# Kernel tuning notes

Hardware: AMD Instinct MI355X
Metric: run time of the kernel (lower is better)

Reference implementation:

```python
import jax, jax.numpy as jnp
import numpy as np

B, T, D, H, MLP, WIN = 4, 2048, 768, 12, 3072, 256
HD = D // H


def setup_inputs() -> dict:
    key = jax.random.key(0)
    ks = jax.random.split(key, 9)
    s = 0.02
    return {
        "x": jax.random.normal(ks[0], (B, T, D), jnp.float32),
        "in_proj_w": jax.random.normal(ks[1], (3 * D, D), jnp.float32) * s,
        "in_proj_b": jax.random.normal(ks[2], (3 * D,), jnp.float32) * s,
        "out_w": jax.random.normal(ks[3], (D, D), jnp.float32) * s,
        "out_b": jax.random.normal(ks[4], (D,), jnp.float32) * s,
        "w1": jax.random.normal(ks[5], (MLP, D), jnp.float32) * s,
        "b1": jax.random.normal(ks[6], (MLP,), jnp.float32) * s,
        "w2": jax.random.normal(ks[7], (D, MLP), jnp.float32) * s,
        "b2": jax.random.normal(ks[8], (D,), jnp.float32) * s,
        "ln1_g": jnp.ones((D,), jnp.float32),
        "ln1_b": jnp.zeros((D,), jnp.float32),
        "ln2_g": jnp.ones((D,), jnp.float32),
        "ln2_b": jnp.zeros((D,), jnp.float32),
        "window_size": WIN,
    }


def _layernorm(v, g, b, eps=1e-5):
    m = v.mean(-1, keepdims=True)
    var = ((v - m) ** 2).mean(-1, keepdims=True)
    return (v - m) / jnp.sqrt(var + eps) * g + b


def reference(x, in_proj_w, in_proj_b, out_w, out_b, w1, b1, w2, b2,
              ln1_g, ln1_b, ln2_g, ln2_b, window_size):
    Bx, Tx, Dx = x.shape
    # --- local (banded) multi-head self-attention on norm1(x) ---
    xn = _layernorm(x, ln1_g, ln1_b)
    qkv = xn @ in_proj_w.T + in_proj_b            # [B,T,3D]
    q, k, v = jnp.split(qkv, 3, axis=-1)
    to_heads = lambda t: t.reshape(Bx, Tx, H, HD).transpose(0, 2, 1, 3)  # [B,H,T,hd]
    q, k, v = to_heads(q), to_heads(k), to_heads(v)
    scale = jnp.asarray(1.0 / np.sqrt(HD), x.dtype)
    scores = jnp.einsum('bhqd,bhkd->bhqk', q, k) * scale  # [B,H,T,T]
    idx = jnp.arange(Tx)
    banned = jnp.abs(idx[:, None] - idx[None, :]) > window_size  # True = masked
    scores = jnp.where(banned, -jnp.inf, scores)
    attn = jax.nn.softmax(scores, axis=-1)
    o = jnp.einsum('bhqk,bhkd->bhqd', attn, v)
    o = o.transpose(0, 2, 1, 3).reshape(Bx, Tx, Dx)
    o = o @ out_w.T + out_b
    x = x + o
    # --- MLP block on norm2(x) ---
    xn = _layernorm(x, ln2_g, ln2_b)
    h = jax.nn.gelu(xn @ w1.T + b1, approximate=False)
    x = x + (h @ w2.T + b2)
    return x
```

## Files before the change

kernel.cpp:

```cpp
#include <hip/hip_runtime.h>
#include <hip/hip_bf16.h>

typedef __bf16 bf16;
typedef __bf16 v8bf __attribute__((ext_vector_type(8)));
typedef __bf16 v4bf __attribute__((ext_vector_type(4)));
typedef float  v4f  __attribute__((ext_vector_type(4)));

#define DEVI __device__ __forceinline__

constexpr int Bc   = 4;
constexpr int Tc   = 2048;
constexpr int Dc   = 768;
constexpr int Hc   = 12;
constexpr int HDc  = 64;
constexpr int MLPc = 3072;
constexpr int QKVc = 2304;
constexpr int BTc  = Bc * Tc;
constexpr int SPAD = 72;

DEVI float b2f(bf16 x) { return (float)x; }
DEVI bf16  f2b(float x) { return (bf16)x; }

#define GLDS(gp, lp) __builtin_amdgcn_global_load_lds( \
    (const __attribute__((address_space(1))) void*)(gp), \
    (__attribute__((address_space(3))) void*)(lp), 16, 0, 0)

__global__ __launch_bounds__(256) void cvt2_kernel(
    const float* __restrict__ s0, bf16* __restrict__ d0, int n0,
    const float* __restrict__ s1, bf16* __restrict__ d1)
{
    int i = blockIdx.x * 256 + threadIdx.x;
    const float* s; bf16* d; int j;
    if (i < n0) { s = s0; d = d0; j = i; }
    else        { s = s1; d = d1; j = i - n0; }
    float4 v = ((const float4*)s)[j];
    v4bf o = { f2b(v.x), f2b(v.y), f2b(v.z), f2b(v.w) };
    ((v4bf*)d)[j] = o;
}

__global__ __launch_bounds__(256) void ln_kernel(
    const float* __restrict__ x, const float* __restrict__ g,
    const float* __restrict__ bt, bf16* __restrict__ out)
{
    const int row = blockIdx.x;
    const int t = threadIdx.x;
    const float* xr = x + (size_t)row * Dc;
    float v[3];
    v[0] = xr[t];
    v[1] = xr[t + 256];
    v[2] = xr[t + 512];
    float s = v[0] + v[1] + v[2];
    float s2 = v[0]*v[0] + v[1]*v[1] + v[2]*v[2];
    #pragma unroll
    for (int off = 32; off > 0; off >>= 1) {
        s  += __shfl_down(s, off);
        s2 += __shfl_down(s2, off);
    }
    __shared__ float red[8];
    const int wave = t >> 6, lane = t & 63;
    if (lane == 0) { red[wave] = s; red[4 + wave] = s2; }
    __syncthreads();
    s  = red[0] + red[1] + red[2] + red[3];
    s2 = red[4] + red[5] + red[6] + red[7];
    const float mean = s * (1.0f / Dc);
    const float var  = s2 * (1.0f / Dc) - mean * mean;
    const float rstd = rsqrtf(var + 1e-5f);
    bf16* orow = out + (size_t)row * Dc;
    #pragma unroll
    for (int i = 0; i < 3; i++) {
        int c = t + i * 256;
        orow[c] = f2b((v[i] - mean) * rstd * g[c] + bt[c]);
    }
}

enum { EPI_QKV = 0, EPI_GELU_BF16 = 1, EPI_RESID_F32 = 2, EPI_ACC_F32 = 3 };

template <int EPI, int TN>
__global__ __launch_bounds__(256) void gemm_bt(
    const bf16* __restrict__ A, const bf16* __restrict__ Bw,
    const float* __restrict__ bias,
    bf16* __restrict__ Cb, float* __restrict__ Cf,
    const float* __restrict__ resf,
    int M, int N, int K, int lda, int ldb)
{
    constexpr int MI = (TN == 128) ? 4 : 2;
    __shared__ __align__(16) bf16 sA[128 * 64];
    __shared__ __align__(16) bf16 sB[TN * 64];
    const int t = threadIdx.x, wave = t >> 6, lane = t & 63;
    const int moff = (TN == 128) ? (wave & 1) * 64 : wave * 32;
    const int noff = (TN == 128) ? (wave >> 1) * 64 : 0;
    const int nx = gridDim.x, ny = gridDim.y;
    const int bid = blockIdx.y * nx + blockIdx.x;
    const int xcd = bid & 7, kk = bid >> 3;
    const int m0 = (xcd * (ny >> 3) + kk / nx) * 128;
    const int n0 = (kk % nx) * TN;
    const bf16* Ag = A + (size_t)m0 * lda;
    const bf16* Bg = Bw + (size_t)n0 * ldb;

    v4f acc[MI][4];
    #pragma unroll
    for (int i = 0; i < MI; i++)
        #pragma unroll
        for (int j = 0; j < 4; j++) acc[i][j] = (v4f)(0.0f);

    for (int k0 = 0; k0 < K; k0 += 64) {
        #pragma unroll
        for (int i = 0; i < 4; i++) {
            int c = i * 256 + t;
            int r = c >> 3, j = (c & 7) ^ (r & 7);
            GLDS(Ag + (size_t)r * lda + k0 + j * 8,
                 &sA[(i * 256 + wave * 64) * 8]);
        }
        #pragma unroll
        for (int i = 0; i < TN / 32; i++) {
            int c = i * 256 + t;
            int r = c >> 3, j = (c & 7) ^ (r & 7);
            GLDS(Bg + (size_t)r * ldb + k0 + j * 8,
                 &sB[(i * 256 + wave * 64) * 8]);
        }
        __syncthreads();
        #pragma unroll
        for (int ks = 0; ks < 2; ks++) {
            const int rq = lane >> 4, rl = lane & 15;
            v8bf a[MI], b[4];
            #pragma unroll
            for (int mi = 0; mi < MI; mi++) {
                const int row = moff + mi * 16 + rl;
                a[mi] = *(const v8bf*)&sA[row * 64 + ((ks * 4 + rq) ^ (row & 7)) * 8];
            }
            #pragma unroll
            for (int ni = 0; ni < 4; ni++) {
                const int row = noff + ni * 16 + rl;
                b[ni] = *(const v8bf*)&sB[row * 64 + ((ks * 4 + rq) ^ (row & 7)) * 8];
            }
            #pragma unroll
            for (int mi = 0; mi < MI; mi++)
                #pragma unroll
                for (int ni = 0; ni < 4; ni++)
                    acc[mi][ni] = __builtin_amdgcn_mfma_f32_16x16x32_bf16(
                        a[mi], b[ni], acc[mi][ni], 0, 0, 0);
        }
        __syncthreads();
    }

    const int rq = lane >> 4, cn = lane & 15;
    #pragma unroll
    for (int mi = 0; mi < MI; mi++)
        #pragma unroll
        for (int ni = 0; ni < 4; ni++) {
            const int col = n0 + noff + ni * 16 + cn;
            const float bv = bias ? bias[col] : 0.0f;
            if constexpr (EPI == EPI_QKV) {
                const int row0 = m0 + moff + mi * 16 + rq * 4;
                if (n0 < 2 * Dc) {
                    bf16* dst = Cb + (col < Dc ? 0 : (size_t)BTc * Dc);
                    const int cadj = col < Dc ? col : col - Dc;
                    #pragma unroll
                    for (int r = 0; r < 4; r++)
                        dst[(size_t)(row0 + r) * Dc + cadj] = f2b(acc[mi][ni][r] + bv);
                } else {
                    const int vcol = col - 2 * Dc;
                    const int hh = vcol >> 6, hd = vcol & 63;
                    const int bb = row0 >> 11, t0 = row0 & 2047;
                    v4bf pk;
                    #pragma unroll
                    for (int r = 0; r < 4; r++) pk[r] = f2b(acc[mi][ni][r] + bv);
                    *(v4bf*)(Cb + 2 * (size_t)BTc * Dc +
                             (((size_t)bb * Hc + hh) * HDc + hd) * Tc + t0) = pk;
                }
            } else {
                #pragma unroll
                for (int r = 0; r < 4; r++) {
                    const int row = m0 + moff + mi * 16 + rq * 4 + r;
                    const size_t idx = (size_t)row * N + col;
                    float vv = acc[mi][ni][r] + bv;
                    if constexpr (EPI == EPI_GELU_BF16) {
                        Cb[idx] = f2b(0.5f * vv * (1.0f + erff(vv * 0.70710678118f)));
                    } else if constexpr (EPI == EPI_RESID_F32) {
                        Cf[idx] = vv + resf[idx];
                    } else {
                        Cf[idx] = vv + Cf[idx];
                    }
                }
            }
        }
}

__global__ __launch_bounds__(256, 2) void attn_kernel(
    const bf16* __restrict__ Qb, const bf16* __restrict__ Kb,
    const bf16* __restrict__ Vt, bf16* __restrict__ o,
    const int* __restrict__ winp)
{
    const int bh = blockIdx.x, qt = blockIdx.y;
    const int b = bh / Hc, h = bh % Hc;
    const int q0 = qt * 64;
    const int win = *winp;
    const int t = threadIdx.x, wave = t >> 6, lane = t & 63;
    const int rq = lane >> 4, cn = lane & 15;
    constexpr float C1 = 0.125f * 1.44269504089f;

    __shared__ __align__(16) bf16 sQ[64 * SPAD];
    __shared__ __align__(16) bf16 sP[4][64 * SPAD];
    __shared__ float sL[4][64], sLf[64];

    const bf16* qp  = Qb + ((size_t)b * Tc + q0) * Dc + h * HDc;
    const bf16* kp  = Kb + ((size_t)b * Tc) * Dc + h * HDc;
    const bf16* vtp = Vt + (size_t)bh * HDc * Tc;

    #pragma unroll
    for (int i = 0; i < 2; i++) {
        int c = i * 256 + t;
        int r = c >> 3, c8 = (c & 7) * 8;
        *(uint4*)&sQ[r * SPAD + c8] = *(const uint4*)(qp + (size_t)r * Dc + c8);
    }
    __syncthreads();

    v4f acc_o[4][4], acc_l[4];
    #pragma unroll
    for (int mi = 0; mi < 4; mi++) {
        acc_l[mi] = (v4f)(0.0f);
        #pragma unroll
        for (int j = 0; j < 4; j++) acc_o[mi][j] = (v4f)(0.0f);
    }
    v8bf vones;
    #pragma unroll
    for (int j = 0; j < 8; j++) vones[j] = f2b(1.0f);

    const int s_lo = (q0 >= win) ? 0 : ((win - q0 + 63) >> 6);
    const int kb_hi = min(Tc - 64, q0 + win);
    const int s_hi = (kb_hi - (q0 - win)) >> 6;

    for (int s = s_lo + wave; s <= s_hi; s += 4) {
        const int kb0 = q0 - win + s * 64;

        v4f sf[4][4];
        #pragma unroll
        for (int mi = 0; mi < 4; mi++)
            #pragma unroll
            for (int ni = 0; ni < 4; ni++) sf[mi][ni] = (v4f)(0.0f);
        #pragma unroll
        for (int ks = 0; ks < 2; ks++) {
            const int kc = ks * 32 + rq * 8;
            v8bf a[4], kf[4];
            #pragma unroll
            for (int mi = 0; mi < 4; mi++)
                a[mi] = *(const v8bf*)&sQ[(mi * 16 + cn) * SPAD + kc];
            #pragma unroll
            for (int ni = 0; ni < 4; ni++)
                kf[ni] = *(const v8bf*)(kp + (size_t)(kb0 + ni * 16 + cn) * Dc + kc);
            #pragma unroll
            for (int mi = 0; mi < 4; mi++)
                #pragma unroll
                for (int ni = 0; ni < 4; ni++)
                    sf[mi][ni] = __builtin_amdgcn_mfma_f32_16x16x32_bf16(
                        a[mi], kf[ni], sf[mi][ni], 0, 0, 0);
        }

        const bool need_mask = (q0 + 63 - kb0 > win) || (kb0 + 63 - q0 > win);
        #pragma unroll
        for (int mi = 0; mi < 4; mi++)
            #pragma unroll
            for (int ni = 0; ni < 4; ni++)
                #pragma unroll
                for (int r = 0; r < 4; r++) {
                    float tt = sf[mi][ni][r] * C1;
                    if (need_mask) {
                        int qi = q0 + mi * 16 + rq * 4 + r;
                        int ki = kb0 + ni * 16 + cn;
                        int dd = qi - ki; dd = dd < 0 ? -dd : dd;
                        tt = (dd > win) ? -INFINITY : tt;
                    }
                    float p = exp2f(fminf(tt, 30.0f));
                    sP[wave][(mi * 16 + rq * 4 + r) * SPAD + ni * 16 + cn] = f2b(p);
                }

        #pragma unroll
        for (int ks = 0; ks < 2; ks++) {
            const int kc = ks * 32 + rq * 8;
            v8bf pa[4], vf[4];
            #pragma unroll
            for (int mi = 0; mi < 4; mi++)
                pa[mi] = *(const v8bf*)&sP[wave][(mi * 16 + cn) * SPAD + kc];
            #pragma unroll
            for (int nh = 0; nh < 4; nh++)
                vf[nh] = *(const v8bf*)(vtp + (size_t)(nh * 16 + cn) * Tc + kb0 + kc);
            #pragma unroll
            for (int mi = 0; mi < 4; mi++)
                acc_l[mi] = __builtin_amdgcn_mfma_f32_16x16x32_bf16(
                    pa[mi], vones, acc_l[mi], 0, 0, 0);
            #pragma unroll
            for (int mi = 0; mi < 4; mi++)
                #pragma unroll
                for (int nh = 0; nh < 4; nh++)
                    acc_o[mi][nh] = __builtin_amdgcn_mfma_f32_16x16x32_bf16(
                        pa[mi], vf[nh], acc_o[mi][nh], 0, 0, 0);
        }
    }

    if (cn == 0) {
        #pragma unroll
        for (int mi = 0; mi < 4; mi++)
            #pragma unroll
            for (int r = 0; r < 4; r++)
                sL[wave][mi * 16 + rq * 4 + r] = acc_l[mi][r];
    }
    __syncthreads();
    float* oacc = (float*)&sP[0][0];
    if (t < 64) {
        float Lv = sL[0][t] + sL[1][t] + sL[2][t] + sL[3][t];
        sLf[t] = (Lv > 0.0f) ? 1.0f / Lv : 0.0f;
    }
    #pragma unroll
    for (int w = 0; w < 4; w++) {
        if (wave == w) {
            #pragma unroll
            for (int mi = 0; mi < 4; mi++)
                #pragma unroll
                for (int r = 0; r < 4; r++) {
                    int row = mi * 16 + rq * 4 + r;
                    #pragma unroll
                    for (int nh = 0; nh < 4; nh++) {
                        float* p = &oacc[row * 64 + nh * 16 + cn];
                        if (w == 0) *p = acc_o[mi][nh][r];
                        else        *p += acc_o[mi][nh][r];
                    }
                }
        }
        __syncthreads();
    }
    bf16* ob = o + ((size_t)b * Tc + q0) * Dc + h * HDc;
    for (int i = t; i < 4096; i += 256) {
        int row = i >> 6, col = i & 63;
        ob[(size_t)row * Dc + col] = f2b(oacc[i] * sLf[row]);
    }
}

extern "C" void kernel_launch(void* const* d_in, const int* in_sizes, int n_in,
                              void* d_out, int out_size, void* d_ws, size_t ws_size,
                              hipStream_t stream)
{
    const float* x     = (const float*)d_in[0];
    const float* inw   = (const float*)d_in[1];
    const float* inb   = (const float*)d_in[2];
    const float* outw  = (const float*)d_in[3];
    const float* outb  = (const float*)d_in[4];
    const float* w1    = (const float*)d_in[5];
    const float* b1    = (const float*)d_in[6];
    const float* w2    = (const float*)d_in[7];
    const float* b2    = (const float*)d_in[8];
    const float* ln1g  = (const float*)d_in[9];
    const float* ln1b  = (const float*)d_in[10];
    const float* ln2g  = (const float*)d_in[11];
    const float* ln2b  = (const float*)d_in[12];
    const int*   winp  = (const int*)d_in[13];
    float* out = (float*)d_out;

    char* ws = (char*)d_ws;
    constexpr size_t A_OFF   = 0;
    constexpr size_t QKV_OFF = (size_t)BTc * Dc * 2;
    constexpr size_t WA_OFF  = QKV_OFF + 3 * (size_t)BTc * Dc * 2;
    constexpr size_t WS_NEED = WA_OFF + (size_t)(QKVc + Dc) * Dc * 2;
    if (ws_size < WS_NEED) return;

    bf16*  xn     = (bf16*)(ws + A_OFF);
    bf16*  qkvb   = (bf16*)(ws + QKV_OFF);
    bf16*  Qb     = qkvb;
    bf16*  Kb     = qkvb + (size_t)BTc * Dc;
    bf16*  Vt     = qkvb + 2 * (size_t)BTc * Dc;
    bf16*  hbuf   = (bf16*)(ws + QKV_OFF);
    bf16*  wmlp   = (bf16*)(ws + QKV_OFF + (size_t)BTc * (2 * Dc) * 2);
    bf16*  w1_b   = wmlp;
    bf16*  w2_b   = wmlp + (size_t)MLPc * Dc;
    bf16*  wqkv_b = (bf16*)(ws + WA_OFF);
    bf16*  wout_b = wqkv_b + (size_t)QKVc * Dc;

    constexpr int HALF = MLPc / 2;
    constexpr int NQKV4 = QKVc * Dc / 4, NOUT4 = Dc * Dc / 4;
    constexpr int NW14  = MLPc * Dc / 4, NW24  = Dc * MLPc / 4;

    cvt2_kernel<<<(NQKV4 + NOUT4) / 256, 256, 0, stream>>>(
        inw, wqkv_b, NQKV4, outw, wout_b);

    ln_kernel<<<BTc, 256, 0, stream>>>(x, ln1g, ln1b, xn);
    gemm_bt<EPI_QKV, 128><<<dim3(QKVc / 128, BTc / 128), 256, 0, stream>>>(
        xn, wqkv_b, inb, qkvb, nullptr, nullptr, BTc, QKVc, Dc, Dc, Dc);
    attn_kernel<<<dim3(Bc * Hc, Tc / 64), 256, 0, stream>>>(Qb, Kb, Vt, xn, winp);
    cvt2_kernel<<<(NW14 + NW24) / 256, 256, 0, stream>>>(
        w1, w1_b, NW14, w2, w2_b);
    gemm_bt<EPI_RESID_F32, 64><<<dim3(Dc / 64, BTc / 128), 256, 0, stream>>>(
        xn, wout_b, outb, nullptr, out, x, BTc, Dc, Dc, Dc, Dc);
    ln_kernel<<<BTc, 256, 0, stream>>>(out, ln2g, ln2b, xn);

    for (int c = 0; c < 2; c++) {
        const bf16* w1c = w1_b + (size_t)c * HALF * Dc;
        const bf16* w2c = w2_b + (size_t)c * HALF;
        gemm_bt<EPI_GELU_BF16, 128><<<dim3(HALF / 128, BTc / 128), 256, 0, stream>>>(
            xn, w1c, b1 + c * HALF, hbuf, nullptr, nullptr, BTc, HALF, Dc, Dc, Dc);
        gemm_bt<EPI_ACC_F32, 64><<<dim3(Dc / 64, BTc / 128), 256, 0, stream>>>(
            hbuf, w2c, (c == 0) ? b2 : nullptr, nullptr, out, nullptr,
            BTc, Dc, HALF, HALF, MLPc);
    }
}
```

Before: 382.8 us.

## Split attention work by query rows per wave and fold softmax scale into Q

Reworks the attention kernel so that each wave owns 16 query rows and loops over all key blocks, instead of splitting key blocks across waves. This removes the cross-wave reduction through shared memory and the block-level barriers. It computes S^T with K as the A operand so that P is written to a small per-wave XOR-swizzled LDS tile. The 1/sqrt(d)*log2e scale is folded into Q in the QKV GEMM epilogue, and launch bounds are raised to allow 4 blocks per CU. The trade-off is that K/V tiles are now reloaded from global memory by each of the four waves, raising redundant global and L2 traffic.

```diff
diff --git a/kernel.cpp b/kernel.cpp
--- a/kernel.cpp
+++ b/kernel.cpp
@@ -16,7 +16,6 @@
 constexpr int MLPc = 3072;
 constexpr int QKVc = 2304;
 constexpr int BTc  = Bc * Tc;
-constexpr int SPAD = 72;
 
 DEVI float b2f(bf16 x) { return (float)x; }
 DEVI bf16  f2b(float x) { return (bf16)x; }
@@ -155,9 +154,10 @@
                 if (n0 < 2 * Dc) {
                     bf16* dst = Cb + (col < Dc ? 0 : (size_t)BTc * Dc);
                     const int cadj = col < Dc ? col : col - Dc;
+                    const float qs = (col < Dc) ? 0.18033688011112042f : 1.0f;
                     #pragma unroll
                     for (int r = 0; r < 4; r++)
-                        dst[(size_t)(row0 + r) * Dc + cadj] = f2b(acc[mi][ni][r] + bv);
+                        dst[(size_t)(row0 + r) * Dc + cadj] = f2b((acc[mi][ni][r] + bv) * qs);
                 } else {
                     const int vcol = col - 2 * Dc;
                     const int hh = vcol >> 6, hd = vcol & 63;
@@ -186,7 +186,7 @@
         }
 }
 
-__global__ __launch_bounds__(256, 2) void attn_kernel(
+__global__ __launch_bounds__(256, 4) void attn_kernel(
     const bf16* __restrict__ Qb, const bf16* __restrict__ Kb,
     const bf16* __restrict__ Vt, bf16* __restrict__ o,
     const int* __restrict__ winp)
@@ -197,31 +197,25 @@
     const int win = *winp;
     const int t = threadIdx.x, wave = t >> 6, lane = t & 63;
     const int rq = lane >> 4, cn = lane & 15;
-    constexpr float C1 = 0.125f * 1.44269504089f;
-
-    __shared__ __align__(16) bf16 sQ[64 * SPAD];
-    __shared__ __align__(16) bf16 sP[4][64 * SPAD];
-    __shared__ float sL[4][64], sLf[64];
-
-    const bf16* qp  = Qb + ((size_t)b * Tc + q0) * Dc + h * HDc;
+    const int qw0 = q0 + wave * 16;
+
+    __shared__ __align__(16) bf16 sP[4][16 * 64];
+    bf16* const sPw = &sP[wave][0];
+    const int swz  = (cn & 7) << 1;
+    const int prow = cn << 6;
+
+    const bf16* qp  = Qb + ((size_t)b * Tc) * Dc + h * HDc;
     const bf16* kp  = Kb + ((size_t)b * Tc) * Dc + h * HDc;
     const bf16* vtp = Vt + (size_t)bh * HDc * Tc;
 
-    #pragma unroll
-    for (int i = 0; i < 2; i++) {
-        int c = i * 256 + t;
-        int r = c >> 3, c8 = (c & 7) * 8;
-        *(uint4*)&sQ[r * SPAD + c8] = *(const uint4*)(qp + (size_t)r * Dc + c8);
-    }
-    __syncthreads();
-
-    v4f acc_o[4][4], acc_l[4];
-    #pragma unroll
-    for (int mi = 0; mi < 4; mi++) {
-        acc_l[mi] = (v4f)(0.0f);
-        #pragma unroll
-        for (int j = 0; j < 4; j++) acc_o[mi][j] = (v4f)(0.0f);
-    }
+    v8bf qf[2];
+    #pragma unroll
+    for (int ks = 0; ks < 2; ks++)
+        qf[ks] = *(const v8bf*)(qp + (size_t)(qw0 + cn) * Dc + ks * 32 + rq * 8);
+
+    v4f acc_o[4], acc_l = (v4f)(0.0f);
+    #pragma unroll
+    for (int nh = 0; nh < 4; nh++) acc_o[nh] = (v4f)(0.0f);
     v8bf vones;
     #pragma unroll
     for (int j = 0; j < 8; j++) vones[j] = f2b(1.0f);
@@ -230,108 +224,66 @@
     const int kb_hi = min(Tc - 64, q0 + win);
     const int s_hi = (kb_hi - (q0 - win)) >> 6;
 
-    for (int s = s_lo + wave; s <= s_hi; s += 4) {
+    for (int s = s_lo; s <= s_hi; s++) {
         const int kb0 = q0 - win + s * 64;
 
-        v4f sf[4][4];
-        #pragma unroll
-        for (int mi = 0; mi < 4; mi++)
-            #pragma unroll
-            for (int ni = 0; ni < 4; ni++) sf[mi][ni] = (v4f)(0.0f);
+        v4f sf[4];
+        #pragma unroll
+        for (int kb = 0; kb < 4; kb++) sf[kb] = (v4f)(0.0f);
         #pragma unroll
         for (int ks = 0; ks < 2; ks++) {
             const int kc = ks * 32 + rq * 8;
-            v8bf a[4], kf[4];
-            #pragma unroll
-            for (int mi = 0; mi < 4; mi++)
-                a[mi] = *(const v8bf*)&sQ[(mi * 16 + cn) * SPAD + kc];
-            #pragma unroll
-            for (int ni = 0; ni < 4; ni++)
-                kf[ni] = *(const v8bf*)(kp + (size_t)(kb0 + ni * 16 + cn) * Dc + kc);
-            #pragma unroll
-            for (int mi = 0; mi < 4; mi++)
-                #pragma unroll
-                for (int ni = 0; ni < 4; ni++)
-                    sf[mi][ni] = __builtin_amdgcn_mfma_f32_16x16x32_bf16(
-                        a[mi], kf[ni], sf[mi][ni], 0, 0, 0);
-        }
-
-        const bool need_mask = (q0 + 63 - kb0 > win) || (kb0 + 63 - q0 > win);
-        #pragma unroll
-        for (int mi = 0; mi < 4; mi++)
-            #pragma unroll
-            for (int ni = 0; ni < 4; ni++)
-                #pragma unroll
-                for (int r = 0; r < 4; r++) {
-                    float tt = sf[mi][ni][r] * C1;
-                    if (need_mask) {
-                        int qi = q0 + mi * 16 + rq * 4 + r;
-                        int ki = kb0 + ni * 16 + cn;
-                        int dd = qi - ki; dd = dd < 0 ? -dd : dd;
-                        tt = (dd > win) ? -INFINITY : tt;
-                    }
-                    float p = exp2f(fminf(tt, 30.0f));
-                    sP[wave][(mi * 16 + rq * 4 + r) * SPAD + ni * 16 + cn] = f2b(p);
+            v8bf kf[4];
+            #pragma unroll
+            for (int kb = 0; kb < 4; kb++)
+                kf[kb] = *(const v8bf*)(kp + (size_t)(kb0 + kb * 16 + cn) * Dc + kc);
+            #pragma unroll
+            for (int kb = 0; kb < 4; kb++)
+                sf[kb] = __builtin_amdgcn_mfma_f32_16x16x32_bf16(
+                    kf[kb], qf[ks], sf[kb], 0, 0, 0);
+        }
+
+        const bool need_mask = (kb0 + 63 - qw0 > win) || (qw0 + 15 - kb0 > win);
+        const int qi = qw0 + cn;
+        #pragma unroll
+        for (int kb = 0; kb < 4; kb++) {
+            v4bf pk;
+            #pragma unroll
+            for (int r = 0; r < 4; r++) {
+                float tt = sf[kb][r];
+                if (need_mask) {
+                    int ki = kb0 + kb * 16 + rq * 4 + r;
+                    int dd = qi - ki; dd = dd < 0 ? -dd : dd;
+                    tt = (dd > win) ? -INFINITY : tt;
                 }
+                pk[r] = f2b(exp2f(fminf(tt, 30.0f)));
+            }
+            *(v4bf*)&sPw[prow + (((kb * 4 + rq) ^ swz) << 2)] = pk;
+        }
 
         #pragma unroll
         for (int ks = 0; ks < 2; ks++) {
             const int kc = ks * 32 + rq * 8;
-            v8bf pa[4], vf[4];
-            #pragma unroll
-            for (int mi = 0; mi < 4; mi++)
-                pa[mi] = *(const v8bf*)&sP[wave][(mi * 16 + cn) * SPAD + kc];
+            v8bf pa = *(const v8bf*)&sPw[prow + (((ks * 8 + rq * 2) ^ swz) << 2)];
+            v8bf vf[4];
             #pragma unroll
             for (int nh = 0; nh < 4; nh++)
                 vf[nh] = *(const v8bf*)(vtp + (size_t)(nh * 16 + cn) * Tc + kb0 + kc);
-            #pragma unroll
-            for (int mi = 0; mi < 4; mi++)
-                acc_l[mi] = __builtin_amdgcn_mfma_f32_16x16x32_bf16(
-                    pa[mi], vones, acc_l[mi], 0, 0, 0);
-            #pragma unroll
-            for (int mi = 0; mi < 4; mi++)
-                #pragma unroll
-                for (int nh = 0; nh < 4; nh++)
-                    acc_o[mi][nh] = __builtin_amdgcn_mfma_f32_16x16x32_bf16(
-                        pa[mi], vf[nh], acc_o[mi][nh], 0, 0, 0);
-        }
-    }
-
-    if (cn == 0) {
-        #pragma unroll
-        for (int mi = 0; mi < 4; mi++)
-            #pragma unroll
-            for (int r = 0; r < 4; r++)
-                sL[wave][mi * 16 + rq * 4 + r] = acc_l[mi][r];
-    }
-    __syncthreads();
-    float* oacc = (float*)&sP[0][0];
-    if (t < 64) {
-        float Lv = sL[0][t] + sL[1][t] + sL[2][t] + sL[3][t];
-        sLf[t] = (Lv > 0.0f) ? 1.0f / Lv : 0.0f;
-    }
-    #pragma unroll
-    for (int w = 0; w < 4; w++) {
-        if (wave == w) {
-            #pragma unroll
-            for (int mi = 0; mi < 4; mi++)
-                #pragma unroll
-                for (int r = 0; r < 4; r++) {
-                    int row = mi * 16 + rq * 4 + r;
-                    #pragma unroll
-                    for (int nh = 0; nh < 4; nh++) {
-                        float* p = &oacc[row * 64 + nh * 16 + cn];
-                        if (w == 0) *p = acc_o[mi][nh][r];
-                        else        *p += acc_o[mi][nh][r];
-                    }
-                }
-        }
-        __syncthreads();
-    }
-    bf16* ob = o + ((size_t)b * Tc + q0) * Dc + h * HDc;
-    for (int i = t; i < 4096; i += 256) {
-        int row = i >> 6, col = i & 63;
-        ob[(size_t)row * Dc + col] = f2b(oacc[i] * sLf[row]);
+            acc_l = __builtin_amdgcn_mfma_f32_16x16x32_bf16(pa, vones, acc_l, 0, 0, 0);
+            #pragma unroll
+            for (int nh = 0; nh < 4; nh++)
+                acc_o[nh] = __builtin_amdgcn_mfma_f32_16x16x32_bf16(
+                    pa, vf[nh], acc_o[nh], 0, 0, 0);
+        }
+    }
+
+    bf16* ob = o + ((size_t)b * Tc + qw0) * Dc + h * HDc;
+    #pragma unroll
+    for (int r = 0; r < 4; r++) {
+        const float invl = 1.0f / acc_l[r];
+        #pragma unroll
+        for (int nh = 0; nh < 4; nh++)
+            ob[(size_t)(rq * 4 + r) * Dc + nh * 16 + cn] = f2b(acc_o[nh][r] * invl);
     }
 }
 
```

Result: slower. 436.9 us (+14.1%).
